# Kernel tuning notes

Hardware: AMD Instinct MI355X
Metric: run time of the kernel (lower is better)

Reference implementation:

```python
import jax, jax.numpy as jnp
import numpy as np

N_HEAD = 16

def setup_inputs() -> dict:
    key = jax.random.key(0)
    ks = jax.random.split(key, 4)
    C = 2048
    x = jax.random.normal(ks[0], (4, 2048, C), dtype=jnp.float32)
    # weights stored [in, out] (transpose of torch Linear's [out, in]); same math y = x @ W + b
    w_qkv = jax.random.normal(ks[1], (C, 3 * C), dtype=jnp.float32) * (1.0 / np.sqrt(C))
    b_qkv = jnp.zeros((3 * C,), dtype=jnp.float32)
    w_proj = jax.random.normal(ks[2], (C, C), dtype=jnp.float32) * (1.0 / np.sqrt(C))
    b_proj = jnp.zeros((C,), dtype=jnp.float32)
    return {"x": x, "w_qkv": w_qkv, "b_qkv": b_qkv, "w_proj": w_proj, "b_proj": b_proj}

def reference(x, w_qkv, b_qkv, w_proj, b_proj):
    B, S, C = x.shape
    H = N_HEAD
    D = C // H
    qkv = x @ w_qkv + b_qkv                      # [B,S,3C]
    q, k, v = jnp.split(qkv, 3, axis=-1)
    # [B,H,S,D]
    q = q.reshape(B, S, H, D).transpose(0, 2, 1, 3)
    k = k.reshape(B, S, H, D).transpose(0, 2, 1, 3)
    v = v.reshape(B, S, H, D).transpose(0, 2, 1, 3)
    scale = 1.0 / np.sqrt(D).astype(np.float32)
    scores = jnp.einsum('bhqd,bhkd->bhqk', q, k) * scale   # [B,H,S,S]
    causal = jnp.tril(jnp.ones((S, S), dtype=bool))
    scores = jnp.where(causal, scores, jnp.finfo(scores.dtype).min)
    attn = jax.nn.softmax(scores, axis=-1)
    y = jnp.einsum('bhqk,bhkd->bhqd', attn, v)              # [B,H,S,D]
    y = y.transpose(0, 2, 1, 3).reshape(B, S, C)
    return y @ w_proj + b_proj
```

## Files before the change

kernel.cpp:

```cpp
#include <hip/hip_runtime.h>
#include <hip/hip_bf16.h>

typedef __bf16 bf16x8 __attribute__((ext_vector_type(8)));
typedef float floatx4 __attribute__((ext_vector_type(4)));

#define LDK 72
#define LDD 136

__device__ __forceinline__ unsigned short f2bf(float f) {
  unsigned u = __float_as_uint(f);
  u += 0x7fffu + ((u >> 16) & 1u);
  return (unsigned short)(u >> 16);
}

__device__ __forceinline__ void async_copy16(const void* g, void* l) {
  __builtin_amdgcn_global_load_lds(
      (const __attribute__((address_space(1))) void*)g,
      (__attribute__((address_space(3))) void*)l, 16, 0, 0);
}

__global__ __launch_bounds__(256) void cvt_bf16(
    const float* __restrict__ in, unsigned short* __restrict__ out) {
  size_t i = ((size_t)blockIdx.x * 256 + threadIdx.x) * 8;
  float4 a0 = *(const float4*)&in[i];
  float4 a1 = *(const float4*)&in[i + 4];
  uint4 d;
  d.x = (unsigned)f2bf(a0.x) | ((unsigned)f2bf(a0.y) << 16);
  d.y = (unsigned)f2bf(a0.z) | ((unsigned)f2bf(a0.w) << 16);
  d.z = (unsigned)f2bf(a1.x) | ((unsigned)f2bf(a1.y) << 16);
  d.w = (unsigned)f2bf(a1.z) | ((unsigned)f2bf(a1.w) << 16);
  *(uint4*)(&out[i]) = d;
}

__global__ __launch_bounds__(256) void transpose_cvt(
    const float* __restrict__ in, unsigned short* __restrict__ out,
    int R, int Ccol) {
  __shared__ unsigned short tile[32][33];
  int c0 = blockIdx.x * 32, r0 = blockIdx.y * 32;
  int tx = threadIdx.x & 31, ty = threadIdx.x >> 5;
  #pragma unroll
  for (int i = 0; i < 32; i += 8)
    tile[ty + i][tx] = f2bf(in[(size_t)(r0 + ty + i) * Ccol + c0 + tx]);
  __syncthreads();
  #pragma unroll
  for (int i = 0; i < 32; i += 8)
    out[(size_t)(c0 + ty + i) * R + r0 + tx] = tile[tx][ty + i];
}

__device__ __forceinline__ void gemm_bt_mainloop(
    const unsigned short* __restrict__ A, const unsigned short* __restrict__ Bt,
    int K, int m0, int n0,
    unsigned short* As, unsigned short* Bs, floatx4 acc[4][4]) {
  const int t = threadIdx.x;
  const int lane = t & 63, w = t >> 6;
  const int wm = w >> 1, wn = w & 1;
  const int l15 = lane & 15, l4 = lane >> 4;
  const int lrow = lane >> 3, lchunk = lane & 7;
  const int gch = lchunk ^ lrow;
  const floatx4 zf = {0.f, 0.f, 0.f, 0.f};
  #pragma unroll
  for (int mi = 0; mi < 4; mi++)
    #pragma unroll
    for (int ni = 0; ni < 4; ni++) acc[mi][ni] = zf;

  for (int k0 = 0; k0 < K; k0 += 64) {
    __syncthreads();
    #pragma unroll
    for (int i = 0; i < 4; i++) {
      int ridx = w * 4 + i;
      int row = ridx * 8 + lrow;
      async_copy16(&A[(size_t)(m0 + row) * K + k0 + gch * 8], &As[ridx * 512]);
    }
    #pragma unroll
    for (int i = 0; i < 4; i++) {
      int ridx = w * 4 + i;
      int row = ridx * 8 + lrow;
      async_copy16(&Bt[(size_t)(n0 + row) * K + k0 + gch * 8], &Bs[ridx * 512]);
    }
    __syncthreads();
    #pragma unroll
    for (int kk = 0; kk < 2; kk++) {
      bf16x8 af[4], bfr[4];
      #pragma unroll
      for (int mi = 0; mi < 4; mi++) {
        int row = wm * 64 + mi * 16 + l15;
        af[mi] = *(const bf16x8*)(&As[row * 64 + ((kk * 4 + l4) ^ (l15 & 7)) * 8]);
      }
      #pragma unroll
      for (int ni = 0; ni < 4; ni++) {
        int row = wn * 64 + ni * 16 + l15;
        bfr[ni] = *(const bf16x8*)(&Bs[row * 64 + ((kk * 4 + l4) ^ (l15 & 7)) * 8]);
      }
      #pragma unroll
      for (int mi = 0; mi < 4; mi++)
        #pragma unroll
        for (int ni = 0; ni < 4; ni++)
          acc[mi][ni] = __builtin_amdgcn_mfma_f32_16x16x32_bf16(
              af[mi], bfr[ni], acc[mi][ni], 0, 0, 0);
    }
  }
}

__global__ __launch_bounds__(256, 3) void gemm_qkv(
    const unsigned short* __restrict__ X, const unsigned short* __restrict__ WT,
    const float* __restrict__ bias,
    unsigned short* __restrict__ Qo, unsigned short* __restrict__ Ko,
    unsigned short* __restrict__ Vto) {
  __shared__ unsigned short As[128 * 64];
  __shared__ unsigned short Bs[128 * 64];
  int n0 = blockIdx.x * 128, m0 = blockIdx.y * 128;
  floatx4 acc[4][4];
  gemm_bt_mainloop(X, WT, 2048, m0, n0, As, Bs, acc);

  const int t = threadIdx.x, lane = t & 63, w = t >> 6;
  const int wm = w >> 1, wn = w & 1;
  const int l15 = lane & 15, l4 = lane >> 4;
  int which = n0 >> 11;
  int h = (n0 & 2047) >> 7;
  int b = m0 >> 11;
  int s0 = m0 & 2047;
  float bv[4];
  #pragma unroll
  for (int ni = 0; ni < 4; ni++)
    bv[ni] = bias[n0 + wn * 64 + ni * 16 + l15];

  if (which < 2) {
    unsigned short* dst = (which == 0) ? Qo : Ko;
    size_t base = (size_t)(b * 16 + h) * 2048;
    #pragma unroll
    for (int mi = 0; mi < 4; mi++)
      #pragma unroll
      for (int ni = 0; ni < 4; ni++) {
        int d = wn * 64 + ni * 16 + l15;
        #pragma unroll
        for (int r = 0; r < 4; r++) {
          int srow = s0 + wm * 64 + mi * 16 + l4 * 4 + r;
          dst[(base + srow) * 128 + d] = f2bf(acc[mi][ni][r] + bv[ni]);
        }
      }
  } else {
    #pragma unroll
    for (int mi = 0; mi < 4; mi++)
      #pragma unroll
      for (int ni = 0; ni < 4; ni++) {
        int d = wn * 64 + ni * 16 + l15;
        int sr = s0 + wm * 64 + mi * 16 + l4 * 4;
        ushort4 v;
        v.x = f2bf(acc[mi][ni][0] + bv[ni]);
        v.y = f2bf(acc[mi][ni][1] + bv[ni]);
        v.z = f2bf(acc[mi][ni][2] + bv[ni]);
        v.w = f2bf(acc[mi][ni][3] + bv[ni]);
        *(ushort4*)(&Vto[((size_t)(b * 16 + h) * 128 + d) * 2048 + sr]) = v;
      }
  }
}

__global__ __launch_bounds__(256, 4) void attn(
    const unsigned short* __restrict__ Qg, const unsigned short* __restrict__ Kg,
    const unsigned short* __restrict__ Vtg, unsigned short* __restrict__ Yg) {
  const int S = 2048, Dh = 128;
  const float c1 = 0.08838834764831845f * 1.4426950408889634f;
  const float NEG_BIG = -3.0e38f;
  __shared__ __bf16 KsPs[64 * LDD];
  __shared__ __bf16 Vs[128 * LDK];
  int qtp = blockIdx.x & 15;
  int bh = blockIdx.x >> 4;
  const int t = threadIdx.x, lane = t & 63, w = t >> 6;
  const int l15 = lane & 15, l4 = lane >> 4;
  const unsigned short* Qb = Qg + (size_t)bh * S * Dh;
  const unsigned short* Kb = Kg + (size_t)bh * S * Dh;
  const unsigned short* Vb = Vtg + (size_t)bh * Dh * S;
  __bf16* Pw = &KsPs[w * 16 * LDK];
  int b = bh >> 4, h = bh & 15;
  const floatx4 zf = {0.f, 0.f, 0.f, 0.f};

  #pragma unroll 1
  for (int half = 0; half < 2; half++) {
    int qt = half ? qtp : (31 - qtp);
    int q0 = qt * 64;
    int qrow_base = q0 + w * 16;
    bf16x8 qf[4];
    #pragma unroll
    for (int kk = 0; kk < 4; kk++)
      qf[kk] = *(const bf16x8*)(
          &Qb[(size_t)(qrow_base + l15) * Dh + kk * 32 + l4 * 8]);
    floatx4 accO[8];
    #pragma unroll
    for (int nd = 0; nd < 8; nd++) accO[nd] = zf;
    float mst[4], lst[4];
    #pragma unroll
    for (int r = 0; r < 4; r++) { mst[r] = NEG_BIG; lst[r] = 0.f; }

    int ntiles = qt + 1;
    #pragma unroll 1
    for (int kt = 0; kt < ntiles; kt++) {
      int k0 = kt * 64;
      __syncthreads();
      #pragma unroll
      for (int i = 0; i < 4; i++) {
        int c = t + i * 256;
        *(uint4*)(&KsPs[(c >> 4) * LDD + (c & 15) * 8]) =
            *(const uint4*)(&Kb[(size_t)(k0 + (c >> 4)) * Dh + (c & 15) * 8]);
      }
      #pragma unroll
      for (int i = 0; i < 4; i++) {
        int c = t + i * 256;
        *(uint4*)(&Vs[(c >> 3) * LDK + (c & 7) * 8]) =
            *(const uint4*)(&Vb[(size_t)(c >> 3) * S + k0 + (c & 7) * 8]);
      }
      __syncthreads();

      floatx4 sc[4];
      #pragma unroll
      for (int ni = 0; ni < 4; ni++) sc[ni] = zf;
      #pragma unroll
      for (int kk = 0; kk < 4; kk++) {
        bf16x8 kf[4];
        #pragma unroll
        for (int ni = 0; ni < 4; ni++)
          kf[ni] = *(const bf16x8*)(&KsPs[(ni * 16 + l15) * LDD + kk * 32 + l4 * 8]);
        #pragma unroll
        for (int ni = 0; ni < 4; ni++)
          sc[ni] = __builtin_amdgcn_mfma_f32_16x16x32_bf16(qf[kk], kf[ni], sc[ni], 0, 0, 0);
      }
      __syncthreads();

      if (kt == qt) {
        #pragma unroll
        for (int ni = 0; ni < 4; ni++)
          #pragma unroll
          for (int r = 0; r < 4; r++)
            if (ni * 16 + l15 > w * 16 + l4 * 4 + r) sc[ni][r] = NEG_BIG;
      }
      float mt[4];
      #pragma unroll
      for (int r = 0; r < 4; r++)
        mt[r] = fmaxf(fmaxf(sc[0][r], sc[1][r]), fmaxf(sc[2][r], sc[3][r]));
      #pragma unroll
      for (int off = 1; off < 16; off <<= 1)
        #pragma unroll
        for (int r = 0; r < 4; r++)
          mt[r] = fmaxf(mt[r], __shfl_xor(mt[r], off, 64));
      float alpha[4], rs[4];
      #pragma unroll
      for (int r = 0; r < 4; r++) {
        float mnew = fmaxf(mst[r], mt[r]);
        alpha[r] = exp2f((mst[r] - mnew) * c1);
        mst[r] = mnew;
        rs[r] = 0.f;
      }
      #pragma unroll
      for (int ni = 0; ni < 4; ni++)
        #pragma unroll
        for (int r = 0; r < 4; r++) {
          float p = exp2f((sc[ni][r] - mst[r]) * c1);
          rs[r] += p;
          Pw[(l4 * 4 + r) * LDK + ni * 16 + l15] = __builtin_bit_cast(__bf16, f2bf(p));
        }
      #pragma unroll
      for (int off = 1; off < 16; off <<= 1)
        #pragma unroll
        for (int r = 0; r < 4; r++)
          rs[r] += __shfl_xor(rs[r], off, 64);
      #pragma unroll
      for (int r = 0; r < 4; r++)
        lst[r] = lst[r] * alpha[r] + rs[r];
      #pragma unroll
      for (int nd = 0; nd < 8; nd++)
        #pragma unroll
        for (int r = 0; r < 4; r++) accO[nd][r] *= alpha[r];
      #pragma unroll
      for (int kk = 0; kk < 2; kk++) {
        bf16x8 pf = *(const bf16x8*)(&Pw[l15 * LDK + kk * 32 + l4 * 8]);
        #pragma unroll
        for (int nd = 0; nd < 8; nd++) {
          bf16x8 vf = *(const bf16x8*)(&Vs[(nd * 16 + l15) * LDK + kk * 32 + l4 * 8]);
          accO[nd] = __builtin_amdgcn_mfma_f32_16x16x32_bf16(pf, vf, accO[nd], 0, 0, 0);
        }
      }
    }
    #pragma unroll
    for (int r = 0; r < 4; r++) {
      float inv = 1.0f / lst[r];
      int srow = qrow_base + l4 * 4 + r;
      size_t rowbase = ((size_t)(b * 2048 + srow)) * 2048 + h * 128;
      #pragma unroll
      for (int nd = 0; nd < 8; nd++)
        Yg[rowbase + nd * 16 + l15] = f2bf(accO[nd][r] * inv);
    }
  }
}

__global__ __launch_bounds__(256, 3) void gemm_proj(
    const unsigned short* __restrict__ Yin, const unsigned short* __restrict__ WT,
    const float* __restrict__ bias, float* __restrict__ Og) {
  __shared__ unsigned short As[128 * 64];
  __shared__ unsigned short Bs[128 * 64];
  int n0 = blockIdx.x * 128, m0 = blockIdx.y * 128;
  floatx4 acc[4][4];
  gemm_bt_mainloop(Yin, WT, 2048, m0, n0, As, Bs, acc);

  const int t = threadIdx.x, lane = t & 63, w = t >> 6;
  const int wm = w >> 1, wn = w & 1;
  const int l15 = lane & 15, l4 = lane >> 4;
  float bv[4];
  #pragma unroll
  for (int ni = 0; ni < 4; ni++)
    bv[ni] = bias[n0 + wn * 64 + ni * 16 + l15];
  #pragma unroll
  for (int mi = 0; mi < 4; mi++)
    #pragma unroll
    for (int ni = 0; ni < 4; ni++)
      #pragma unroll
      for (int r = 0; r < 4; r++)
        Og[(size_t)(m0 + wm * 64 + mi * 16 + l4 * 4 + r) * 2048 +
           n0 + wn * 64 + ni * 16 + l15] = acc[mi][ni][r] + bv[ni];
}

extern "C" void kernel_launch(void* const* d_in, const int* in_sizes, int n_in,
                              void* d_out, int out_size, void* d_ws, size_t ws_size,
                              hipStream_t stream) {
  const float* x      = (const float*)d_in[0];
  const float* w_qkv  = (const float*)d_in[1];
  const float* b_qkv  = (const float*)d_in[2];
  const float* w_proj = (const float*)d_in[3];
  const float* b_proj = (const float*)d_in[4];
  float* out = (float*)d_out;
  char* ws = (char*)d_ws;

  unsigned short* Q   = (unsigned short*)d_out;
  unsigned short* Kt  = (unsigned short*)((char*)d_out + 33554432);
  unsigned short* Vt  = (unsigned short*)(ws);
  unsigned short* Xbf = (unsigned short*)(ws + 33554432);
  unsigned short* Y   = (unsigned short*)(ws + 33554432);
  unsigned short* WqT = (unsigned short*)(ws + 67108864);
  unsigned short* WpT = (unsigned short*)(ws + 67108864);

  cvt_bf16<<<dim3(8192), 256, 0, stream>>>(x, Xbf);
  transpose_cvt<<<dim3(192, 64), 256, 0, stream>>>(w_qkv, WqT, 2048, 6144);
  gemm_qkv<<<dim3(48, 64), 256, 0, stream>>>(Xbf, WqT, b_qkv, Q, Kt, Vt);
  attn<<<dim3(1024), 256, 0, stream>>>(Q, Kt, Vt, Y);
  transpose_cvt<<<dim3(64, 64), 256, 0, stream>>>(w_proj, WpT, 2048, 2048);
  gemm_proj<<<dim3(16, 64), 256, 0, stream>>>(Y, WpT, b_proj, out);
}
```

Baseline: 647.1 us.

## Double-buffer K/V tiles with async global-to-LDS copies and XOR swizzle

```diff
diff --git a/kernel.cpp b/kernel.cpp
--- a/kernel.cpp
+++ b/kernel.cpp
@@ -5,7 +5,6 @@
 typedef float floatx4 __attribute__((ext_vector_type(4)));
 
 #define LDK 72
-#define LDD 136
 
 __device__ __forceinline__ unsigned short f2bf(float f) {
   unsigned u = __float_as_uint(f);
@@ -155,22 +154,47 @@
   }
 }
 
-__global__ __launch_bounds__(256, 4) void attn(
+__device__ __forceinline__ void attn_stage(
+    const unsigned short* __restrict__ Kb, const unsigned short* __restrict__ Vb,
+    __bf16* Ksel, __bf16* Vsel, int k0, int lane, int w) {
+  const int krow_in = lane >> 4, kch = lane & 15;
+  const int vrow_in = lane >> 3, vch = lane & 7;
+  #pragma unroll
+  for (int u = 0; u < 4; u++) {
+    int uk = w * 4 + u;
+    int row = uk * 4 + krow_in;
+    int sch = kch ^ (row & 7);
+    async_copy16(&Kb[(size_t)(k0 + row) * 128 + sch * 8], Ksel + uk * 512);
+  }
+  #pragma unroll
+  for (int u = 0; u < 4; u++) {
+    int uv = w * 4 + u;
+    int row = uv * 8 + vrow_in;
+    int sch = vch ^ vrow_in;
+    async_copy16(&Vb[(size_t)row * 2048 + k0 + sch * 8], Vsel + uv * 512);
+  }
+}
+
+__global__ __launch_bounds__(256, 2) void attn(
     const unsigned short* __restrict__ Qg, const unsigned short* __restrict__ Kg,
     const unsigned short* __restrict__ Vtg, unsigned short* __restrict__ Yg) {
   const int S = 2048, Dh = 128;
   const float c1 = 0.08838834764831845f * 1.4426950408889634f;
   const float NEG_BIG = -3.0e38f;
-  __shared__ __bf16 KsPs[64 * LDD];
-  __shared__ __bf16 Vs[128 * LDK];
-  int qtp = blockIdx.x & 15;
-  int bh = blockIdx.x >> 4;
+  __shared__ __bf16 Ks[2][64 * 128];
+  __shared__ __bf16 Vs[2][128 * 64];
+  __shared__ __bf16 Pl[4][16 * LDK];
+
+  int wg = blockIdx.x;
+  int lg = (wg & 7) * 128 + (wg >> 3);
+  int qtp = lg & 15;
+  int bh = lg >> 4;
   const int t = threadIdx.x, lane = t & 63, w = t >> 6;
   const int l15 = lane & 15, l4 = lane >> 4;
   const unsigned short* Qb = Qg + (size_t)bh * S * Dh;
   const unsigned short* Kb = Kg + (size_t)bh * S * Dh;
   const unsigned short* Vb = Vtg + (size_t)bh * Dh * S;
-  __bf16* Pw = &KsPs[w * 16 * LDK];
+  __bf16* Pw = Pl[w];
   int b = bh >> 4, h = bh & 15;
   const floatx4 zf = {0.f, 0.f, 0.f, 0.f};
 
@@ -192,24 +216,17 @@
     for (int r = 0; r < 4; r++) { mst[r] = NEG_BIG; lst[r] = 0.f; }
 
     int ntiles = qt + 1;
+    int cur = 0;
+    attn_stage(Kb, Vb, Ks[0], Vs[0], 0, lane, w);
+    __syncthreads();
+
     #pragma unroll 1
     for (int kt = 0; kt < ntiles; kt++) {
-      int k0 = kt * 64;
-      __syncthreads();
-      #pragma unroll
-      for (int i = 0; i < 4; i++) {
-        int c = t + i * 256;
-        *(uint4*)(&KsPs[(c >> 4) * LDD + (c & 15) * 8]) =
-            *(const uint4*)(&Kb[(size_t)(k0 + (c >> 4)) * Dh + (c & 15) * 8]);
-      }
-      #pragma unroll
-      for (int i = 0; i < 4; i++) {
-        int c = t + i * 256;
-        *(uint4*)(&Vs[(c >> 3) * LDK + (c & 7) * 8]) =
-            *(const uint4*)(&Vb[(size_t)(c >> 3) * S + k0 + (c & 7) * 8]);
-      }
-      __syncthreads();
-
+      if (kt + 1 < ntiles)
+        attn_stage(Kb, Vb, Ks[cur ^ 1], Vs[cur ^ 1], (kt + 1) * 64, lane, w);
+
+      const __bf16* Kcur = Ks[cur];
+      const __bf16* Vcur = Vs[cur];
       floatx4 sc[4];
       #pragma unroll
       for (int ni = 0; ni < 4; ni++) sc[ni] = zf;
@@ -217,13 +234,15 @@
       for (int kk = 0; kk < 4; kk++) {
         bf16x8 kf[4];
         #pragma unroll
-        for (int ni = 0; ni < 4; ni++)
-          kf[ni] = *(const bf16x8*)(&KsPs[(ni * 16 + l15) * LDD + kk * 32 + l4 * 8]);
+        for (int ni = 0; ni < 4; ni++) {
+          int row = ni * 16 + l15;
+          kf[ni] = *(const bf16x8*)(
+              &Kcur[row * 128 + (((kk * 4 + l4) ^ (l15 & 7)) << 3)]);
+        }
         #pragma unroll
         for (int ni = 0; ni < 4; ni++)
           sc[ni] = __builtin_amdgcn_mfma_f32_16x16x32_bf16(qf[kk], kf[ni], sc[ni], 0, 0, 0);
       }
-      __syncthreads();
 
       if (kt == qt) {
         #pragma unroll
@@ -274,10 +293,14 @@
         bf16x8 pf = *(const bf16x8*)(&Pw[l15 * LDK + kk * 32 + l4 * 8]);
         #pragma unroll
         for (int nd = 0; nd < 8; nd++) {
-          bf16x8 vf = *(const bf16x8*)(&Vs[(nd * 16 + l15) * LDK + kk * 32 + l4 * 8]);
+          int row = nd * 16 + l15;
+          bf16x8 vf = *(const bf16x8*)(
+              &Vcur[row * 64 + (((kk * 4 + l4) ^ (l15 & 7)) << 3)]);
           accO[nd] = __builtin_amdgcn_mfma_f32_16x16x32_bf16(pf, vf, accO[nd], 0, 0, 0);
         }
       }
+      __syncthreads();
+      cur ^= 1;
     }
     #pragma unroll
     for (int r = 0; r < 4; r++) {
```

Result: faster. 626.7 us (-3.2%).
